# Optimization experiments

Hardware: AMD Instinct MI355X
Metric: run time of the kernel (lower is better)

## Reference

```python
import jax, jax.numpy as jnp
import numpy as np

IN, OUT, H = 512, 128, 128
B = 131072


def setup_inputs() -> dict:
    key = jax.random.key(0)
    ks = jax.random.split(key, 16)
    s = 0.05
    return {
        "x": jax.random.normal(ks[0], (B, IN), dtype=jnp.float32),
        # DNN params
        "fc1_w": jax.random.normal(ks[1], (128, IN), dtype=jnp.float32) * s,
        "fc1_b": jnp.zeros((128,), jnp.float32),
        "fc2_w": jax.random.normal(ks[2], (64, 128), dtype=jnp.float32) * s,
        "fc2_b": jnp.zeros((64,), jnp.float32),
        "fc3_w": jax.random.normal(ks[3], (OUT, 64), dtype=jnp.float32) * s,
        "fc3_b": jnp.zeros((OUT,), jnp.float32),
        # LSTM params (PyTorch gate order: i, f, g, o)
        "W_ih": jax.random.normal(ks[4], (4 * H, IN + OUT), dtype=jnp.float32) * s,
        "W_hh": jax.random.normal(ks[5], (4 * H, H), dtype=jnp.float32) * s,
        "b_ih": jnp.zeros((4 * H,), jnp.float32),
        "b_hh": jnp.zeros((4 * H,), jnp.float32),
        # Attention + final FC
        "attn_w": jax.random.normal(ks[6], (1, H), dtype=jnp.float32) * s,
        "attn_b": jnp.zeros((1,), jnp.float32),
        "fc_w": jax.random.normal(ks[7], (OUT, H), dtype=jnp.float32) * s,
        "fc_b": jnp.zeros((OUT,), jnp.float32),
    }


def reference(x, fc1_w, fc1_b, fc2_w, fc2_b, fc3_w, fc3_b,
              W_ih, W_hh, b_ih, b_hh, attn_w, attn_b, fc_w, fc_b):
    # DNN branch
    d = jax.nn.relu(x @ fc1_w.T + fc1_b)
    d = jax.nn.relu(d @ fc2_w.T + fc2_b)
    d = d @ fc3_w.T + fc3_b                     # [B, OUT]
    xc = jnp.concatenate([x, d], axis=1)        # [B, IN+OUT]
    # Single-step LSTM with h0 = c0 = 0 (W_hh contributes nothing but biases kept)
    gates = xc @ W_ih.T + b_ih + b_hh           # [B, 4H]
    i, f, g, o = jnp.split(gates, 4, axis=1)
    c = jax.nn.sigmoid(i) * jnp.tanh(g)         # f*c0 = 0
    h = jax.nn.sigmoid(o) * jnp.tanh(c)         # [B, H]
    lstm_out = h[:, None, :]                    # [B, 1, H]
    # Attention over seq_len=1 (softmax over a single score == 1)
    scores = jnp.squeeze(lstm_out @ attn_w.T + attn_b, axis=2)  # [B, 1]
    w = jax.nn.softmax(scores, axis=1)
    ctx = jnp.einsum('bs,bsh->bh', w, lstm_out)  # [B, H]
    return ctx @ fc_w.T + fc_b                   # [B, OUT]
```

## Files before the change

kernel.cpp:

```cpp
#include <hip/hip_runtime.h>
#include <hip/hip_bf16.h>

typedef __attribute__((ext_vector_type(8))) short bf16x8;
typedef __attribute__((ext_vector_type(4))) float f32x4;
typedef __attribute__((ext_vector_type(4))) short s16x4;
typedef unsigned short ushort_t;

__device__ __forceinline__ unsigned short f2bf(float f) {
    unsigned int u = __float_as_uint(f);
    u = (u + 0x7FFFu + ((u >> 16) & 1u)) >> 16;
    return (unsigned short)u;
}
__device__ __forceinline__ float fast_sigmoid(float x) {
    return 1.0f / (1.0f + __expf(-x));
}
__device__ __forceinline__ float fast_tanh(float x) {
    x = fminf(fmaxf(x, -15.0f), 15.0f);
    float e = __expf(2.0f * x);
    return (e - 1.0f) / (e + 1.0f);
}
__device__ __forceinline__ f32x4 mfma16(bf16x8 a, bf16x8 b, f32x4 c) {
    return __builtin_amdgcn_mfma_f32_16x16x32_bf16(a, b, c, 0, 0, 0);
}

__global__ void convert_w_kernel(const float* __restrict__ w1, const float* __restrict__ w2,
                                 const float* __restrict__ w3, const float* __restrict__ wih,
                                 const float* __restrict__ fcw, ushort_t* __restrict__ outw) {
    int i = blockIdx.x * 256 + threadIdx.x;
    float v;
    if (i < 65536)       v = w1[i];
    else if (i < 73728)  v = w2[i - 65536];
    else if (i < 81920)  v = w3[i - 73728];
    else if (i < 409600) v = wih[i - 81920];
    else                 v = fcw[i - 409600];
    outw[i] = f2bf(v);
}

#define XS_LD 520
#define D1_LD 136
#define D2_LD 72
#define D3_LD 136
#define HS_LD 136

__global__ __launch_bounds__(512, 2) void fused_mlp_lstm_kernel(
    const float* __restrict__ x,
    const float* __restrict__ b1, const float* __restrict__ b2, const float* __restrict__ b3,
    const float* __restrict__ b_ih, const float* __restrict__ b_hh,
    const float* __restrict__ fc_b,
    const ushort_t* __restrict__ wbf,
    float* __restrict__ out)
{
    __shared__ ushort_t sm[64 * (XS_LD + D1_LD + D2_LD + D3_LD + HS_LD)];
    ushort_t* xs  = sm;
    ushort_t* d1s = xs  + 64 * XS_LD;
    ushort_t* d2s = d1s + 64 * D1_LD;
    ushort_t* d3s = d2s + 64 * D2_LD;
    ushort_t* hs  = d3s + 64 * D3_LD;

    const ushort_t* W1  = wbf;
    const ushort_t* W2  = wbf + 65536;
    const ushort_t* W3  = wbf + 73728;
    const ushort_t* WIH = wbf + 81920;
    const ushort_t* FCW = wbf + 409600;

    const int t  = threadIdx.x;
    const int w  = t >> 6;
    const int l  = t & 63;
    const int q  = l >> 4;
    const int lm = l & 15;
    const int ko = q * 8;
    const int n0 = w * 16;
    const long rowBase = (long)blockIdx.x * 64;

    bf16x8 bw1[16];
    #pragma unroll
    for (int kk = 0; kk < 16; ++kk)
        bw1[kk] = *(const bf16x8*)(W1 + (n0 + lm) * 512 + kk * 32 + ko);

    const float4* xv = (const float4*)(x + rowBase * 512);
    #pragma unroll
    for (int i = 0; i < 8; ++i) {
        int u = t + i * 512;
        int row = u >> 6, c4 = u & 63;
        float4 v = xv[row * 128 + c4];
        s16x4 pk;
        pk.x = (short)f2bf(v.x); pk.y = (short)f2bf(v.y);
        pk.z = (short)f2bf(v.z); pk.w = (short)f2bf(v.w);
        *(s16x4*)(xs + row * XS_LD + c4 * 4) = pk;
    }
    __syncthreads();

    float4 vb[8];
    #pragma unroll
    for (int i = 0; i < 8; ++i) {
        int u = t + i * 512;
        vb[i] = xv[(u >> 6) * 128 + 64 + (u & 63)];
    }

    f32x4 a1[4] = {{0,0,0,0},{0,0,0,0},{0,0,0,0},{0,0,0,0}};
    #pragma unroll
    for (int kk = 0; kk < 8; ++kk) {
        #pragma unroll
        for (int s = 0; s < 4; ++s) {
            bf16x8 fa = *(const bf16x8*)(xs + (s * 16 + lm) * XS_LD + kk * 32 + ko);
            a1[s] = mfma16(fa, bw1[kk], a1[s]);
        }
    }

    #pragma unroll
    for (int i = 0; i < 8; ++i) {
        int u = t + i * 512;
        int row = u >> 6, c4 = u & 63;
        s16x4 pk;
        pk.x = (short)f2bf(vb[i].x); pk.y = (short)f2bf(vb[i].y);
        pk.z = (short)f2bf(vb[i].z); pk.w = (short)f2bf(vb[i].w);
        *(s16x4*)(xs + row * XS_LD + (64 + c4) * 4) = pk;
    }
    __syncthreads();

    #pragma unroll
    for (int kk = 8; kk < 16; ++kk) {
        #pragma unroll
        for (int s = 0; s < 4; ++s) {
            bf16x8 fa = *(const bf16x8*)(xs + (s * 16 + lm) * XS_LD + kk * 32 + ko);
            a1[s] = mfma16(fa, bw1[kk], a1[s]);
        }
    }
    {
        float bv = b1[n0 + lm];
        #pragma unroll
        for (int s = 0; s < 4; ++s)
            #pragma unroll
            for (int r = 0; r < 4; ++r)
                d1s[(s * 16 + q * 4 + r) * D1_LD + n0 + lm] = f2bf(fmaxf(a1[s][r] + bv, 0.0f));
    }

    const int w4 = w & 3, half = w >> 2;
    const int n2 = w4 * 16;
    bf16x8 bw2[4];
    #pragma unroll
    for (int kk = 0; kk < 4; ++kk)
        bw2[kk] = *(const bf16x8*)(W2 + (n2 + lm) * 128 + kk * 32 + ko);
    __syncthreads();

    {
        f32x4 a2[2] = {{0,0,0,0},{0,0,0,0}};
        #pragma unroll
        for (int kk = 0; kk < 4; ++kk) {
            #pragma unroll
            for (int s = 0; s < 2; ++s) {
                bf16x8 fa = *(const bf16x8*)(d1s + (half * 32 + s * 16 + lm) * D1_LD + kk * 32 + ko);
                a2[s] = mfma16(fa, bw2[kk], a2[s]);
            }
        }
        float bv = b2[n2 + lm];
        #pragma unroll
        for (int s = 0; s < 2; ++s)
            #pragma unroll
            for (int r = 0; r < 4; ++r)
                d2s[(half * 32 + s * 16 + q * 4 + r) * D2_LD + n2 + lm] = f2bf(fmaxf(a2[s][r] + bv, 0.0f));
    }

    const int rI = n0, rG = 256 + n0, rO = 384 + n0;
    bf16x8 bw3[2];
    #pragma unroll
    for (int kk = 0; kk < 2; ++kk)
        bw3[kk] = *(const bf16x8*)(W3 + (n0 + lm) * 64 + kk * 32 + ko);
    bf16x8 bi0[8], bg0[8], bo0[8];
    #pragma unroll
    for (int j = 0; j < 8; ++j) {
        bi0[j] = *(const bf16x8*)(WIH + (rI + lm) * 640 + j * 32 + ko);
        bg0[j] = *(const bf16x8*)(WIH + (rG + lm) * 640 + j * 32 + ko);
        bo0[j] = *(const bf16x8*)(WIH + (rO + lm) * 640 + j * 32 + ko);
    }
    __syncthreads();

    {
        f32x4 a3[4] = {{0,0,0,0},{0,0,0,0},{0,0,0,0},{0,0,0,0}};
        #pragma unroll
        for (int kk = 0; kk < 2; ++kk) {
            #pragma unroll
            for (int s = 0; s < 4; ++s) {
                bf16x8 fa = *(const bf16x8*)(d2s + (s * 16 + lm) * D2_LD + kk * 32 + ko);
                a3[s] = mfma16(fa, bw3[kk], a3[s]);
            }
        }
        float bv = b3[n0 + lm];
        #pragma unroll
        for (int s = 0; s < 4; ++s)
            #pragma unroll
            for (int r = 0; r < 4; ++r)
                d3s[(s * 16 + q * 4 + r) * D3_LD + n0 + lm] = f2bf(a3[s][r] + bv);
    }

    f32x4 aI[4] = {{0,0,0,0},{0,0,0,0},{0,0,0,0},{0,0,0,0}};
    f32x4 aG[4] = {{0,0,0,0},{0,0,0,0},{0,0,0,0},{0,0,0,0}};
    f32x4 aO[4] = {{0,0,0,0},{0,0,0,0},{0,0,0,0},{0,0,0,0}};
    #pragma unroll
    for (int j = 0; j < 8; ++j) {
        bf16x8 fa[4];
        #pragma unroll
        for (int s = 0; s < 4; ++s)
            fa[s] = *(const bf16x8*)(xs + (s * 16 + lm) * XS_LD + j * 32 + ko);
        #pragma unroll
        for (int s = 0; s < 4; ++s) {
            aI[s] = mfma16(fa[s], bi0[j], aI[s]);
            aG[s] = mfma16(fa[s], bg0[j], aG[s]);
            aO[s] = mfma16(fa[s], bo0[j], aO[s]);
        }
    }
    {
        bf16x8 bi1[8], bg1[8], bo1[8];
        #pragma unroll
        for (int j = 0; j < 8; ++j) {
            bi1[j] = *(const bf16x8*)(WIH + (rI + lm) * 640 + (8 + j) * 32 + ko);
            bg1[j] = *(const bf16x8*)(WIH + (rG + lm) * 640 + (8 + j) * 32 + ko);
            bo1[j] = *(const bf16x8*)(WIH + (rO + lm) * 640 + (8 + j) * 32 + ko);
        }
        #pragma unroll
        for (int j = 0; j < 8; ++j) {
            bf16x8 fa[4];
            #pragma unroll
            for (int s = 0; s < 4; ++s)
                fa[s] = *(const bf16x8*)(xs + (s * 16 + lm) * XS_LD + (8 + j) * 32 + ko);
            #pragma unroll
            for (int s = 0; s < 4; ++s) {
                aI[s] = mfma16(fa[s], bi1[j], aI[s]);
                aG[s] = mfma16(fa[s], bg1[j], aG[s]);
                aO[s] = mfma16(fa[s], bo1[j], aO[s]);
            }
        }
    }
    {
        bf16x8 biB[4], bgB[4], boB[4];
        #pragma unroll
        for (int j = 0; j < 4; ++j) {
            biB[j] = *(const bf16x8*)(WIH + (rI + lm) * 640 + 512 + j * 32 + ko);
            bgB[j] = *(const bf16x8*)(WIH + (rG + lm) * 640 + 512 + j * 32 + ko);
            boB[j] = *(const bf16x8*)(WIH + (rO + lm) * 640 + 512 + j * 32 + ko);
        }
        __syncthreads();
        #pragma unroll
        for (int j = 0; j < 4; ++j) {
            bf16x8 fa[4];
            #pragma unroll
            for (int s = 0; s < 4; ++s)
                fa[s] = *(const bf16x8*)(d3s + (s * 16 + lm) * D3_LD + j * 32 + ko);
            #pragma unroll
            for (int s = 0; s < 4; ++s) {
                aI[s] = mfma16(fa[s], biB[j], aI[s]);
                aG[s] = mfma16(fa[s], bgB[j], aG[s]);
                aO[s] = mfma16(fa[s], boB[j], aO[s]);
            }
        }
    }
    {
        float biasI = b_ih[rI + lm] + b_hh[rI + lm];
        float biasG = b_ih[rG + lm] + b_hh[rG + lm];
        float biasO = b_ih[rO + lm] + b_hh[rO + lm];
        #pragma unroll
        for (int s = 0; s < 4; ++s)
            #pragma unroll
            for (int r = 0; r < 4; ++r) {
                float c = fast_sigmoid(aI[s][r] + biasI) * fast_tanh(aG[s][r] + biasG);
                float h = fast_sigmoid(aO[s][r] + biasO) * fast_tanh(c);
                hs[(s * 16 + q * 4 + r) * HS_LD + n0 + lm] = f2bf(h);
            }
    }
    bf16x8 bw5[4];
    #pragma unroll
    for (int kk = 0; kk < 4; ++kk)
        bw5[kk] = *(const bf16x8*)(FCW + (n0 + lm) * 128 + kk * 32 + ko);
    __syncthreads();

    {
        f32x4 a5[4] = {{0,0,0,0},{0,0,0,0},{0,0,0,0},{0,0,0,0}};
        #pragma unroll
        for (int kk = 0; kk < 4; ++kk) {
            #pragma unroll
            for (int s = 0; s < 4; ++s) {
                bf16x8 fa = *(const bf16x8*)(hs + (s * 16 + lm) * HS_LD + kk * 32 + ko);
                a5[s] = mfma16(fa, bw5[kk], a5[s]);
            }
        }
        float bv = fc_b[n0 + lm];
        #pragma unroll
        for (int s = 0; s < 4; ++s)
            #pragma unroll
            for (int r = 0; r < 4; ++r)
                out[(rowBase + s * 16 + q * 4 + r) * 128 + n0 + lm] = a5[s][r] + bv;
    }
}

extern "C" void kernel_launch(void* const* d_in, const int* in_sizes, int n_in,
                              void* d_out, int out_size, void* d_ws, size_t ws_size,
                              hipStream_t stream) {
    const float* x    = (const float*)d_in[0];
    const float* w1   = (const float*)d_in[1];
    const float* b1   = (const float*)d_in[2];
    const float* w2   = (const float*)d_in[3];
    const float* b2   = (const float*)d_in[4];
    const float* w3   = (const float*)d_in[5];
    const float* b3   = (const float*)d_in[6];
    const float* wih  = (const float*)d_in[7];
    const float* b_ih = (const float*)d_in[9];
    const float* b_hh = (const float*)d_in[10];
    const float* fcw  = (const float*)d_in[13];
    const float* fcb  = (const float*)d_in[14];

    ushort_t* wbf = (ushort_t*)d_ws;
    float* out = (float*)d_out;

    convert_w_kernel<<<1664, 256, 0, stream>>>(w1, w2, w3, wih, fcw, wbf);
    fused_mlp_lstm_kernel<<<131072 / 64, 512, 0, stream>>>(
        x, b1, b2, b3, b_ih, b_hh, fcb, wbf, out);
}
```

Before: 577.6 us.

## Halve rows per block, alias shared buffers, and stream weights to raise occupancy

Each block now handles 32 rows instead of 64, and the grid is doubled to match. Shared memory is shrunk by reusing the xs and d1 regions for the later h and d3 buffers. LSTM weight fragments are loaded in small chunks rather than held in large register arrays, and launch bounds now request 6 blocks per CU instead of 2. The aim is higher occupancy to hide the latency of the memory-bound x reads, at the cost of loading each weight fragment twice as often per row processed.

```diff
diff --git a/kernel.cpp b/kernel.cpp
--- a/kernel.cpp
+++ b/kernel.cpp
@@ -42,7 +42,7 @@
 #define D3_LD 136
 #define HS_LD 136
 
-__global__ __launch_bounds__(512, 2) void fused_mlp_lstm_kernel(
+__global__ __launch_bounds__(512, 6) void fused_mlp_lstm_kernel(
     const float* __restrict__ x,
     const float* __restrict__ b1, const float* __restrict__ b2, const float* __restrict__ b3,
     const float* __restrict__ b_ih, const float* __restrict__ b_hh,
@@ -50,12 +50,12 @@
     const ushort_t* __restrict__ wbf,
     float* __restrict__ out)
 {
-    __shared__ ushort_t sm[64 * (XS_LD + D1_LD + D2_LD + D3_LD + HS_LD)];
+    __shared__ ushort_t sm[32 * (XS_LD + D1_LD + D2_LD)];
     ushort_t* xs  = sm;
-    ushort_t* d1s = xs  + 64 * XS_LD;
-    ushort_t* d2s = d1s + 64 * D1_LD;
-    ushort_t* d3s = d2s + 64 * D2_LD;
-    ushort_t* hs  = d3s + 64 * D3_LD;
+    ushort_t* d1s = xs  + 32 * XS_LD;
+    ushort_t* d2s = d1s + 32 * D1_LD;
+    ushort_t* d3s = d1s;
+    ushort_t* hs  = xs;
 
     const ushort_t* W1  = wbf;
     const ushort_t* W2  = wbf + 65536;
@@ -70,16 +70,16 @@
     const int lm = l & 15;
     const int ko = q * 8;
     const int n0 = w * 16;
-    const long rowBase = (long)blockIdx.x * 64;
-
-    bf16x8 bw1[16];
-    #pragma unroll
-    for (int kk = 0; kk < 16; ++kk)
-        bw1[kk] = *(const bf16x8*)(W1 + (n0 + lm) * 512 + kk * 32 + ko);
+    const long rowBase = (long)blockIdx.x * 32;
+
+    bf16x8 bw1a[8];
+    #pragma unroll
+    for (int kk = 0; kk < 8; ++kk)
+        bw1a[kk] = *(const bf16x8*)(W1 + (n0 + lm) * 512 + kk * 32 + ko);
 
     const float4* xv = (const float4*)(x + rowBase * 512);
     #pragma unroll
-    for (int i = 0; i < 8; ++i) {
+    for (int i = 0; i < 4; ++i) {
         int u = t + i * 512;
         int row = u >> 6, c4 = u & 63;
         float4 v = xv[row * 128 + c4];
@@ -90,25 +90,25 @@
     }
     __syncthreads();
 
-    float4 vb[8];
-    #pragma unroll
-    for (int i = 0; i < 8; ++i) {
+    float4 vb[4];
+    #pragma unroll
+    for (int i = 0; i < 4; ++i) {
         int u = t + i * 512;
         vb[i] = xv[(u >> 6) * 128 + 64 + (u & 63)];
     }
 
-    f32x4 a1[4] = {{0,0,0,0},{0,0,0,0},{0,0,0,0},{0,0,0,0}};
+    f32x4 a1[2] = {{0,0,0,0},{0,0,0,0}};
     #pragma unroll
     for (int kk = 0; kk < 8; ++kk) {
         #pragma unroll
-        for (int s = 0; s < 4; ++s) {
+        for (int s = 0; s < 2; ++s) {
             bf16x8 fa = *(const bf16x8*)(xs + (s * 16 + lm) * XS_LD + kk * 32 + ko);
-            a1[s] = mfma16(fa, bw1[kk], a1[s]);
-        }
-    }
-
-    #pragma unroll
-    for (int i = 0; i < 8; ++i) {
+            a1[s] = mfma16(fa, bw1a[kk], a1[s]);
+        }
+    }
+
+    #pragma unroll
+    for (int i = 0; i < 4; ++i) {
         int u = t + i * 512;
         int row = u >> 6, c4 = u & 63;
         s16x4 pk;
@@ -116,20 +116,25 @@
         pk.z = (short)f2bf(vb[i].z); pk.w = (short)f2bf(vb[i].w);
         *(s16x4*)(xs + row * XS_LD + (64 + c4) * 4) = pk;
     }
-    __syncthreads();
-
-    #pragma unroll
-    for (int kk = 8; kk < 16; ++kk) {
-        #pragma unroll
-        for (int s = 0; s < 4; ++s) {
-            bf16x8 fa = *(const bf16x8*)(xs + (s * 16 + lm) * XS_LD + kk * 32 + ko);
-            a1[s] = mfma16(fa, bw1[kk], a1[s]);
+
+    bf16x8 bw1b[8];
+    #pragma unroll
+    for (int kk = 0; kk < 8; ++kk)
+        bw1b[kk] = *(const bf16x8*)(W1 + (n0 + lm) * 512 + (8 + kk) * 32 + ko);
+    __syncthreads();
+
+    #pragma unroll
+    for (int kk = 0; kk < 8; ++kk) {
+        #pragma unroll
+        for (int s = 0; s < 2; ++s) {
+            bf16x8 fa = *(const bf16x8*)(xs + (s * 16 + lm) * XS_LD + (8 + kk) * 32 + ko);
+            a1[s] = mfma16(fa, bw1b[kk], a1[s]);
         }
     }
     {
         float bv = b1[n0 + lm];
         #pragma unroll
-        for (int s = 0; s < 4; ++s)
+        for (int s = 0; s < 2; ++s)
             #pragma unroll
             for (int r = 0; r < 4; ++r)
                 d1s[(s * 16 + q * 4 + r) * D1_LD + n0 + lm] = f2bf(fmaxf(a1[s][r] + bv, 0.0f));
@@ -144,21 +149,16 @@
     __syncthreads();
 
     {
-        f32x4 a2[2] = {{0,0,0,0},{0,0,0,0}};
+        f32x4 a2 = {0,0,0,0};
         #pragma unroll
         for (int kk = 0; kk < 4; ++kk) {
-            #pragma unroll
-            for (int s = 0; s < 2; ++s) {
-                bf16x8 fa = *(const bf16x8*)(d1s + (half * 32 + s * 16 + lm) * D1_LD + kk * 32 + ko);
-                a2[s] = mfma16(fa, bw2[kk], a2[s]);
-            }
+            bf16x8 fa = *(const bf16x8*)(d1s + (half * 16 + lm) * D1_LD + kk * 32 + ko);
+            a2 = mfma16(fa, bw2[kk], a2);
         }
         float bv = b2[n2 + lm];
         #pragma unroll
-        for (int s = 0; s < 2; ++s)
-            #pragma unroll
-            for (int r = 0; r < 4; ++r)
-                d2s[(half * 32 + s * 16 + q * 4 + r) * D2_LD + n2 + lm] = f2bf(fmaxf(a2[s][r] + bv, 0.0f));
+        for (int r = 0; r < 4; ++r)
+            d2s[(half * 16 + q * 4 + r) * D2_LD + n2 + lm] = f2bf(fmaxf(a2[r] + bv, 0.0f));
     }
 
     const int rI = n0, rG = 256 + n0, rO = 384 + n0;
@@ -166,9 +166,9 @@
     #pragma unroll
     for (int kk = 0; kk < 2; ++kk)
         bw3[kk] = *(const bf16x8*)(W3 + (n0 + lm) * 64 + kk * 32 + ko);
-    bf16x8 bi0[8], bg0[8], bo0[8];
-    #pragma unroll
-    for (int j = 0; j < 8; ++j) {
+    bf16x8 bi0[2], bg0[2], bo0[2];
+    #pragma unroll
+    for (int j = 0; j < 2; ++j) {
         bi0[j] = *(const bf16x8*)(WIH + (rI + lm) * 640 + j * 32 + ko);
         bg0[j] = *(const bf16x8*)(WIH + (rG + lm) * 640 + j * 32 + ko);
         bo0[j] = *(const bf16x8*)(WIH + (rO + lm) * 640 + j * 32 + ko);
@@ -176,90 +176,115 @@
     __syncthreads();
 
     {
-        f32x4 a3[4] = {{0,0,0,0},{0,0,0,0},{0,0,0,0},{0,0,0,0}};
+        f32x4 a3[2] = {{0,0,0,0},{0,0,0,0}};
         #pragma unroll
         for (int kk = 0; kk < 2; ++kk) {
             #pragma unroll
-            for (int s = 0; s < 4; ++s) {
+            for (int s = 0; s < 2; ++s) {
                 bf16x8 fa = *(const bf16x8*)(d2s + (s * 16 + lm) * D2_LD + kk * 32 + ko);
                 a3[s] = mfma16(fa, bw3[kk], a3[s]);
             }
         }
         float bv = b3[n0 + lm];
         #pragma unroll
-        for (int s = 0; s < 4; ++s)
+        for (int s = 0; s < 2; ++s)
             #pragma unroll
             for (int r = 0; r < 4; ++r)
                 d3s[(s * 16 + q * 4 + r) * D3_LD + n0 + lm] = f2bf(a3[s][r] + bv);
     }
 
-    f32x4 aI[4] = {{0,0,0,0},{0,0,0,0},{0,0,0,0},{0,0,0,0}};
-    f32x4 aG[4] = {{0,0,0,0},{0,0,0,0},{0,0,0,0},{0,0,0,0}};
-    f32x4 aO[4] = {{0,0,0,0},{0,0,0,0},{0,0,0,0},{0,0,0,0}};
-    #pragma unroll
-    for (int j = 0; j < 8; ++j) {
-        bf16x8 fa[4];
-        #pragma unroll
-        for (int s = 0; s < 4; ++s)
+    f32x4 aI[2] = {{0,0,0,0},{0,0,0,0}};
+    f32x4 aG[2] = {{0,0,0,0},{0,0,0,0}};
+    f32x4 aO[2] = {{0,0,0,0},{0,0,0,0}};
+    #pragma unroll
+    for (int j = 0; j < 2; ++j) {
+        bf16x8 fa[2];
+        #pragma unroll
+        for (int s = 0; s < 2; ++s)
             fa[s] = *(const bf16x8*)(xs + (s * 16 + lm) * XS_LD + j * 32 + ko);
         #pragma unroll
-        for (int s = 0; s < 4; ++s) {
+        for (int s = 0; s < 2; ++s) {
             aI[s] = mfma16(fa[s], bi0[j], aI[s]);
             aG[s] = mfma16(fa[s], bg0[j], aG[s]);
             aO[s] = mfma16(fa[s], bo0[j], aO[s]);
         }
     }
-    {
-        bf16x8 bi1[8], bg1[8], bo1[8];
-        #pragma unroll
-        for (int j = 0; j < 8; ++j) {
-            bi1[j] = *(const bf16x8*)(WIH + (rI + lm) * 640 + (8 + j) * 32 + ko);
-            bg1[j] = *(const bf16x8*)(WIH + (rG + lm) * 640 + (8 + j) * 32 + ko);
-            bo1[j] = *(const bf16x8*)(WIH + (rO + lm) * 640 + (8 + j) * 32 + ko);
-        }
-        #pragma unroll
-        for (int j = 0; j < 8; ++j) {
-            bf16x8 fa[4];
-            #pragma unroll
-            for (int s = 0; s < 4; ++s)
-                fa[s] = *(const bf16x8*)(xs + (s * 16 + lm) * XS_LD + (8 + j) * 32 + ko);
-            #pragma unroll
-            for (int s = 0; s < 4; ++s) {
-                aI[s] = mfma16(fa[s], bi1[j], aI[s]);
-                aG[s] = mfma16(fa[s], bg1[j], aG[s]);
-                aO[s] = mfma16(fa[s], bo1[j], aO[s]);
-            }
-        }
-    }
-    {
-        bf16x8 biB[4], bgB[4], boB[4];
-        #pragma unroll
-        for (int j = 0; j < 4; ++j) {
+    #pragma unroll
+    for (int c = 1; c < 8; ++c) {
+        bf16x8 bi[2], bg[2], bo[2];
+        #pragma unroll
+        for (int j2 = 0; j2 < 2; ++j2) {
+            int j = c * 2 + j2;
+            bi[j2] = *(const bf16x8*)(WIH + (rI + lm) * 640 + j * 32 + ko);
+            bg[j2] = *(const bf16x8*)(WIH + (rG + lm) * 640 + j * 32 + ko);
+            bo[j2] = *(const bf16x8*)(WIH + (rO + lm) * 640 + j * 32 + ko);
+        }
+        #pragma unroll
+        for (int j2 = 0; j2 < 2; ++j2) {
+            int j = c * 2 + j2;
+            bf16x8 fa[2];
+            #pragma unroll
+            for (int s = 0; s < 2; ++s)
+                fa[s] = *(const bf16x8*)(xs + (s * 16 + lm) * XS_LD + j * 32 + ko);
+            #pragma unroll
+            for (int s = 0; s < 2; ++s) {
+                aI[s] = mfma16(fa[s], bi[j2], aI[s]);
+                aG[s] = mfma16(fa[s], bg[j2], aG[s]);
+                aO[s] = mfma16(fa[s], bo[j2], aO[s]);
+            }
+        }
+    }
+
+    {
+        bf16x8 biB[2], bgB[2], boB[2];
+        #pragma unroll
+        for (int j = 0; j < 2; ++j) {
             biB[j] = *(const bf16x8*)(WIH + (rI + lm) * 640 + 512 + j * 32 + ko);
             bgB[j] = *(const bf16x8*)(WIH + (rG + lm) * 640 + 512 + j * 32 + ko);
             boB[j] = *(const bf16x8*)(WIH + (rO + lm) * 640 + 512 + j * 32 + ko);
         }
         __syncthreads();
         #pragma unroll
-        for (int j = 0; j < 4; ++j) {
-            bf16x8 fa[4];
-            #pragma unroll
-            for (int s = 0; s < 4; ++s)
+        for (int j = 0; j < 2; ++j) {
+            bf16x8 fa[2];
+            #pragma unroll
+            for (int s = 0; s < 2; ++s)
                 fa[s] = *(const bf16x8*)(d3s + (s * 16 + lm) * D3_LD + j * 32 + ko);
             #pragma unroll
-            for (int s = 0; s < 4; ++s) {
+            for (int s = 0; s < 2; ++s) {
                 aI[s] = mfma16(fa[s], biB[j], aI[s]);
                 aG[s] = mfma16(fa[s], bgB[j], aG[s]);
                 aO[s] = mfma16(fa[s], boB[j], aO[s]);
             }
         }
-    }
+        bf16x8 biB2[2], bgB2[2], boB2[2];
+        #pragma unroll
+        for (int j = 0; j < 2; ++j) {
+            biB2[j] = *(const bf16x8*)(WIH + (rI + lm) * 640 + 512 + (2 + j) * 32 + ko);
+            bgB2[j] = *(const bf16x8*)(WIH + (rG + lm) * 640 + 512 + (2 + j) * 32 + ko);
+            boB2[j] = *(const bf16x8*)(WIH + (rO + lm) * 640 + 512 + (2 + j) * 32 + ko);
+        }
+        #pragma unroll
+        for (int j = 0; j < 2; ++j) {
+            bf16x8 fa[2];
+            #pragma unroll
+            for (int s = 0; s < 2; ++s)
+                fa[s] = *(const bf16x8*)(d3s + (s * 16 + lm) * D3_LD + (2 + j) * 32 + ko);
+            #pragma unroll
+            for (int s = 0; s < 2; ++s) {
+                aI[s] = mfma16(fa[s], biB2[j], aI[s]);
+                aG[s] = mfma16(fa[s], bgB2[j], aG[s]);
+                aO[s] = mfma16(fa[s], boB2[j], aO[s]);
+            }
+        }
+    }
+
     {
         float biasI = b_ih[rI + lm] + b_hh[rI + lm];
         float biasG = b_ih[rG + lm] + b_hh[rG + lm];
         float biasO = b_ih[rO + lm] + b_hh[rO + lm];
         #pragma unroll
-        for (int s = 0; s < 4; ++s)
+        for (int s = 0; s < 2; ++s)
             #pragma unroll
             for (int r = 0; r < 4; ++r) {
                 float c = fast_sigmoid(aI[s][r] + biasI) * fast_tanh(aG[s][r] + biasG);
@@ -274,18 +299,18 @@
     __syncthreads();
 
     {
-        f32x4 a5[4] = {{0,0,0,0},{0,0,0,0},{0,0,0,0},{0,0,0,0}};
+        f32x4 a5[2] = {{0,0,0,0},{0,0,0,0}};
         #pragma unroll
         for (int kk = 0; kk < 4; ++kk) {
             #pragma unroll
-            for (int s = 0; s < 4; ++s) {
+            for (int s = 0; s < 2; ++s) {
                 bf16x8 fa = *(const bf16x8*)(hs + (s * 16 + lm) * HS_LD + kk * 32 + ko);
                 a5[s] = mfma16(fa, bw5[kk], a5[s]);
             }
         }
         float bv = fc_b[n0 + lm];
         #pragma unroll
-        for (int s = 0; s < 4; ++s)
+        for (int s = 0; s < 2; ++s)
             #pragma unroll
             for (int r = 0; r < 4; ++r)
                 out[(rowBase + s * 16 + q * 4 + r) * 128 + n0 + lm] = a5[s][r] + bv;
@@ -312,6 +337,6 @@
     float* out = (float*)d_out;
 
     convert_w_kernel<<<1664, 256, 0, stream>>>(w1, w2, w3, wih, fcw, wbf);
-    fused_mlp_lstm_kernel<<<131072 / 64, 512, 0, stream>>>(
+    fused_mlp_lstm_kernel<<<131072 / 32, 512, 0, stream>>>(
         x, b1, b2, b3, b_ih, b_hh, fcb, wbf, out);
 }
```

Measured after the change: 648.6 us. 1.12x slower.
